# Kernel optimization log

Hardware: AMD Instinct MI355X
Metric: run time of the kernel (lower is better)

Reference implementation:

```python
import jax, jax.numpy as jnp
import numpy as np

B = 8192  # number of covariance matrices
N = 64    # n_assets


def setup_inputs() -> dict:
    key = jax.random.key(0)
    A = jax.random.normal(key, (B, N, N), dtype=jnp.float32)
    # SPD covariance: A A^T / N + 0.1 I  (real covariances are SPD)
    sigma = jnp.einsum('bij,bkj->bik', A, A) / N + 0.1 * jnp.eye(N, dtype=jnp.float32)
    return {"sigma": sigma}


def reference(sigma) -> jnp.ndarray:
    # Symmetrize, as the original does: 0.5 * (S + S^T)
    sym = 0.5 * (sigma + jnp.swapaxes(sigma, -1, -2))  # [B, N, N]
    n = sym.shape[-1]
    ones = jnp.ones((*sym.shape[:-2], n), dtype=sym.dtype)  # [B, N]
    # Closed-form min-variance (short selling allowed): w = S^-1 1 / (1^T S^-1 1)
    z = jnp.linalg.solve(sym, ones[..., None])[..., 0]      # [B, N]
    w = z / jnp.sum(z, axis=-1, keepdims=True)              # [B, N]
    return w[..., None]  # [B, N, 1], matching expand_dims(axis=-1)
```

## Files before the change

### kernel.cpp

```cpp
#include <hip/hip_runtime.h>


#define NN 64

typedef float v2f __attribute__((ext_vector_type(2)));
typedef float v4f __attribute__((ext_vector_type(4)));

template <int I> struct ic { static constexpr int value = I; };

template <int Start, int End, typename F>
__device__ __forceinline__ void static_for(F&& f) {
    if constexpr (Start < End) {
        f(ic<Start>{});
        static_for<Start + 1, End>(static_cast<F&&>(f));
    }
}

__device__ __forceinline__ float rlane(float v, int lane) {
    return __int_as_float(__builtin_amdgcn_readlane(__float_as_int(v), lane));
}

__device__ __forceinline__ float frcp(float x) {
#if __has_builtin(__builtin_amdgcn_rcpf)
    return __builtin_amdgcn_rcpf(x);
#else
    return 1.0f / x;
#endif
}

__device__ __forceinline__ v2f fma2(v2f a, v2f b, v2f c) {
#if __has_builtin(__builtin_elementwise_fma)
    return __builtin_elementwise_fma(a, b, c);
#else
    v2f r; r.x = fmaf(a.x, b.x, c.x); r.y = fmaf(a.y, b.y, c.y); return r;
#endif
}

__global__
__attribute__((amdgpu_flat_work_group_size(256, 256), amdgpu_waves_per_eu(3, 3)))
void minvar_kernel(const float* __restrict__ sigma,
                   float* __restrict__ out,
                   int batch) {
    __shared__ float pb[4][2][2 * NN * 4 / 2];

    const int lane = threadIdx.x & 63;
    const int wid  = threadIdx.x >> 6;
    const int bid  = blockIdx.x * 4 + wid;
    if (bid >= batch) return;

    const float* __restrict__ p = sigma + (size_t)bid * (NN * NN) + (size_t)lane * NN;

    v2f r[NN / 2];
    static_for<0, NN / 4>([&](auto j4c) {
        constexpr int j4 = decltype(j4c)::value;
        v4f v = reinterpret_cast<const v4f*>(p)[j4];
        r[2 * j4 + 0] = v2f{v.x, v.y};
        r[2 * j4 + 1] = v2f{v.z, v.w};
    });

    float b = 1.0f;
    float d = 1.0f;
    const int wbase = (lane >> 1) * 8 + (lane & 1);

    static_for<0, 16>([&](auto pc) {
        constexpr int P  = decltype(pc)::value;
        constexpr int k0 = 4 * P;
        constexpr int m0 = 2 * P;
        float* __restrict__ wb = &pb[wid][P & 1][0];

        const float el0  = r[m0].x;
        if constexpr (P < 15) wb[wbase + 0] = el0;
        const float piv0 = rlane(el0, k0);
        const float nf0  = (lane != k0) ? (-el0 * frcp(piv0)) : 0.0f;
        d = (lane == k0) ? el0 : d;
        b = fmaf(nf0, rlane(b, k0), b);
        const float u01 = rlane(r[m0].y,     k0);
        const float u02 = rlane(r[m0 + 1].x, k0);
        const float u03 = rlane(r[m0 + 1].y, k0);
        r[m0].y     = fmaf(nf0, u01, r[m0].y);
        r[m0 + 1].x = fmaf(nf0, u02, r[m0 + 1].x);
        r[m0 + 1].y = fmaf(nf0, u03, r[m0 + 1].y);

        const float el1  = r[m0].y;
        if constexpr (P < 15) wb[wbase + 2] = el1;
        const float piv1 = rlane(el1, k0 + 1);
        const float nf1  = (lane != k0 + 1) ? (-el1 * frcp(piv1)) : 0.0f;
        d = (lane == k0 + 1) ? el1 : d;
        b = fmaf(nf1, rlane(b, k0 + 1), b);
        const float u12 = rlane(r[m0 + 1].x, k0 + 1);
        const float u13 = rlane(r[m0 + 1].y, k0 + 1);
        r[m0 + 1].x = fmaf(nf1, u12, r[m0 + 1].x);
        r[m0 + 1].y = fmaf(nf1, u13, r[m0 + 1].y);

        const float el2  = r[m0 + 1].x;
        if constexpr (P < 15) wb[wbase + 4] = el2;
        const float piv2 = rlane(el2, k0 + 2);
        const float nf2  = (lane != k0 + 2) ? (-el2 * frcp(piv2)) : 0.0f;
        d = (lane == k0 + 2) ? el2 : d;
        b = fmaf(nf2, rlane(b, k0 + 2), b);
        const float u23 = rlane(r[m0 + 1].y, k0 + 2);
        r[m0 + 1].y = fmaf(nf2, u23, r[m0 + 1].y);

        const float el3  = r[m0 + 1].y;
        if constexpr (P < 15) wb[wbase + 6] = el3;
        const float piv3 = rlane(el3, k0 + 3);
        const float nf3  = (lane != k0 + 3) ? (-el3 * frcp(piv3)) : 0.0f;
        d = (lane == k0 + 3) ? el3 : d;
        b = fmaf(nf3, rlane(b, k0 + 3), b);

        if constexpr (P < 15) {
            const v2f n0 = v2f{nf0, nf0}, n1 = v2f{nf1, nf1};
            const v2f n2 = v2f{nf2, nf2}, n3 = v2f{nf3, nf3};
            static_for<0, 4>([&](auto gc) {
                constexpr int G = decltype(gc)::value;
                constexpr int s = m0 + 2 + 8 * G;
                if constexpr (s < NN / 2) {
                    constexpr int e = (s + 8 < NN / 2) ? (s + 8) : (NN / 2);
                    v4f lo[4], hi[4];
                    static_for<s, e>([&](auto mc) {
                        constexpr int m = decltype(mc)::value;
                        constexpr int q = m - s;
                        if constexpr (q < 4) {
                            lo[q] = *reinterpret_cast<const v4f*>(wb + 8 * m);
                            hi[q] = *reinterpret_cast<const v4f*>(wb + 8 * m + 4);
                        }
                    });
                    static_for<s, e>([&](auto mc) {
                        constexpr int m = decltype(mc)::value;
                        constexpr int q = m - s;
                        if constexpr (q >= 4) {
                            constexpr int j0 = 2 * m, j1 = 2 * m + 1;
                            float ax = r[m].x, ay = r[m].y;
                            ax = fmaf(nf0, rlane(el0, j0), ax);
                            ay = fmaf(nf0, rlane(el0, j1), ay);
                            ax = fmaf(nf1, rlane(el1, j0), ax);
                            ay = fmaf(nf1, rlane(el1, j1), ay);
                            ax = fmaf(nf2, rlane(el2, j0), ax);
                            ay = fmaf(nf2, rlane(el2, j1), ay);
                            ax = fmaf(nf3, rlane(el3, j0), ax);
                            ay = fmaf(nf3, rlane(el3, j1), ay);
                            r[m] = v2f{ax, ay};
                        }
                    });
                    static_for<s, e>([&](auto mc) {
                        constexpr int m = decltype(mc)::value;
                        constexpr int q = m - s;
                        if constexpr (q < 4) {
                            v2f acc = r[m];
                            acc = fma2(n0, v2f{lo[q].x, lo[q].y}, acc);
                            acc = fma2(n1, v2f{lo[q].z, lo[q].w}, acc);
                            acc = fma2(n2, v2f{hi[q].x, hi[q].y}, acc);
                            acc = fma2(n3, v2f{hi[q].z, hi[q].w}, acc);
                            r[m] = acc;
                        }
                    });
                }
            });
        }
    });

    const float z = b * frcp(d);

    float tot = z;
    #pragma unroll
    for (int off = 32; off >= 1; off >>= 1)
        tot += __shfl_xor(tot, off, 64);

    out[(size_t)bid * NN + lane] = z * frcp(tot);
}

extern "C" void kernel_launch(void* const* d_in, const int* in_sizes, int n_in,
                              void* d_out, int out_size, void* d_ws, size_t ws_size,
                              hipStream_t stream) {
    const float* sigma = (const float*)d_in[0];
    float* out = (float*)d_out;
    const int batch  = in_sizes[0] / (NN * NN);
    const int blocks = (batch + 3) / 4;
    minvar_kernel<<<blocks, 256, 0, stream>>>(sigma, out, batch);
}
```

Measured before the change: 193.9 us.

## Defer trailing-column updates of each panel into next panel's pivot steps

After each 4-column panel, only the next panel's columns (m0+2..m0+7) are updated immediately. The remaining trailing columns are updated during the following panel's serial pivot chain, using saved multipliers and the double-buffered LDS panel. This aims to hide the latency of the dependent pivot/readlane chain behind independent FMA work. The cost is more live registers (saved el/nf values) and a more complex schedule that could spill or hurt occupancy.

```diff
diff --git a/kernel.cpp b/kernel.cpp
--- a/kernel.cpp
+++ b/kernel.cpp
@@ -62,11 +62,63 @@
     float d = 1.0f;
     const int wbase = (lane >> 1) * 8 + (lane & 1);
 
+    float el0p = 0.f, el1p = 0.f, el2p = 0.f, el3p = 0.f;
+    float nf0p = 0.f, nf1p = 0.f, nf2p = 0.f, nf3p = 0.f;
+
     static_for<0, 16>([&](auto pc) {
         constexpr int P  = decltype(pc)::value;
         constexpr int k0 = 4 * P;
         constexpr int m0 = 2 * P;
-        float* __restrict__ wb = &pb[wid][P & 1][0];
+        float* __restrict__ wb  = &pb[wid][P & 1][0];
+        float* __restrict__ wbp = &pb[wid][(P & 1) ^ 1][0];
+
+        auto do_rest_group = [&](auto Gc) {
+            constexpr int G = decltype(Gc)::value;
+            constexpr int s = 2 * P + 6 + 8 * G;
+            if constexpr (P >= 1 && s < NN / 2) {
+                constexpr int e = (s + 8 < NN / 2) ? (s + 8) : (NN / 2);
+                const v2f n0 = v2f{nf0p, nf0p}, n1 = v2f{nf1p, nf1p};
+                const v2f n2 = v2f{nf2p, nf2p}, n3 = v2f{nf3p, nf3p};
+                v4f lo[4], hi[4];
+                static_for<s, e>([&](auto mc) {
+                    constexpr int m = decltype(mc)::value;
+                    constexpr int q = m - s;
+                    if constexpr (q < 4) {
+                        lo[q] = *reinterpret_cast<const v4f*>(wbp + 8 * m);
+                        hi[q] = *reinterpret_cast<const v4f*>(wbp + 8 * m + 4);
+                    }
+                });
+                static_for<s, e>([&](auto mc) {
+                    constexpr int m = decltype(mc)::value;
+                    constexpr int q = m - s;
+                    if constexpr (q >= 4) {
+                        constexpr int j0 = 2 * m, j1 = 2 * m + 1;
+                        float ax = r[m].x, ay = r[m].y;
+                        ax = fmaf(nf0p, rlane(el0p, j0), ax);
+                        ay = fmaf(nf0p, rlane(el0p, j1), ay);
+                        ax = fmaf(nf1p, rlane(el1p, j0), ax);
+                        ay = fmaf(nf1p, rlane(el1p, j1), ay);
+                        ax = fmaf(nf2p, rlane(el2p, j0), ax);
+                        ay = fmaf(nf2p, rlane(el2p, j1), ay);
+                        ax = fmaf(nf3p, rlane(el3p, j0), ax);
+                        ay = fmaf(nf3p, rlane(el3p, j1), ay);
+                        r[m] = v2f{ax, ay};
+                    }
+                });
+                static_for<s, e>([&](auto mc) {
+                    constexpr int m = decltype(mc)::value;
+                    constexpr int q = m - s;
+                    if constexpr (q < 4) {
+                        v2f acc = r[m];
+                        acc = fma2(n0, v2f{lo[q].x, lo[q].y}, acc);
+                        acc = fma2(n1, v2f{lo[q].z, lo[q].w}, acc);
+                        acc = fma2(n2, v2f{hi[q].x, hi[q].y}, acc);
+                        acc = fma2(n3, v2f{hi[q].z, hi[q].w}, acc);
+                        r[m] = acc;
+                    }
+                });
+            }
+        };
 
         const float el0  = r[m0].x;
         if constexpr (P < 15) wb[wbase + 0] = el0;
@@ -81,6 +133,8 @@
         r[m0 + 1].x = fmaf(nf0, u02, r[m0 + 1].x);
         r[m0 + 1].y = fmaf(nf0, u03, r[m0 + 1].y);
 
+        do_rest_group(ic<0>{});
+
         const float el1  = r[m0].y;
         if constexpr (P < 15) wb[wbase + 2] = el1;
         const float piv1 = rlane(el1, k0 + 1);
@@ -92,6 +146,8 @@
         r[m0 + 1].x = fmaf(nf1, u12, r[m0 + 1].x);
         r[m0 + 1].y = fmaf(nf1, u13, r[m0 + 1].y);
 
+        do_rest_group(ic<1>{});
+
         const float el2  = r[m0 + 1].x;
         if constexpr (P < 15) wb[wbase + 4] = el2;
         const float piv2 = rlane(el2, k0 + 2);
@@ -101,6 +157,8 @@
         const float u23 = rlane(r[m0 + 1].y, k0 + 2);
         r[m0 + 1].y = fmaf(nf2, u23, r[m0 + 1].y);
 
+        do_rest_group(ic<2>{});
+
         const float el3  = r[m0 + 1].y;
         if constexpr (P < 15) wb[wbase + 6] = el3;
         const float piv3 = rlane(el3, k0 + 3);
@@ -109,53 +167,50 @@
         b = fmaf(nf3, rlane(b, k0 + 3), b);
 
         if constexpr (P < 15) {
+            constexpr int s0 = m0 + 2;
+            constexpr int e0 = (m0 + 8 < NN / 2) ? (m0 + 8) : (NN / 2);
             const v2f n0 = v2f{nf0, nf0}, n1 = v2f{nf1, nf1};
             const v2f n2 = v2f{nf2, nf2}, n3 = v2f{nf3, nf3};
-            static_for<0, 4>([&](auto gc) {
-                constexpr int G = decltype(gc)::value;
-                constexpr int s = m0 + 2 + 8 * G;
-                if constexpr (s < NN / 2) {
-                    constexpr int e = (s + 8 < NN / 2) ? (s + 8) : (NN / 2);
-                    v4f lo[4], hi[4];
-                    static_for<s, e>([&](auto mc) {
-                        constexpr int m = decltype(mc)::value;
-                        constexpr int q = m - s;
-                        if constexpr (q < 4) {
-                            lo[q] = *reinterpret_cast<const v4f*>(wb + 8 * m);
-                            hi[q] = *reinterpret_cast<const v4f*>(wb + 8 * m + 4);
-                        }
-                    });
-                    static_for<s, e>([&](auto mc) {
-                        constexpr int m = decltype(mc)::value;
-                        constexpr int q = m - s;
-                        if constexpr (q >= 4) {
-                            constexpr int j0 = 2 * m, j1 = 2 * m + 1;
-                            float ax = r[m].x, ay = r[m].y;
-                            ax = fmaf(nf0, rlane(el0, j0), ax);
-                            ay = fmaf(nf0, rlane(el0, j1), ay);
-                            ax = fmaf(nf1, rlane(el1, j0), ax);
-                            ay = fmaf(nf1, rlane(el1, j1), ay);
-                            ax = fmaf(nf2, rlane(el2, j0), ax);
-                            ay = fmaf(nf2, rlane(el2, j1), ay);
-                            ax = fmaf(nf3, rlane(el3, j0), ax);
-                            ay = fmaf(nf3, rlane(el3, j1), ay);
-                            r[m] = v2f{ax, ay};
-                        }
-                    });
-                    static_for<s, e>([&](auto mc) {
-                        constexpr int m = decltype(mc)::value;
-                        constexpr int q = m - s;
-                        if constexpr (q < 4) {
-                            v2f acc = r[m];
-                            acc = fma2(n0, v2f{lo[q].x, lo[q].y}, acc);
-                            acc = fma2(n1, v2f{lo[q].z, lo[q].w}, acc);
-                            acc = fma2(n2, v2f{hi[q].x, hi[q].y}, acc);
-                            acc = fma2(n3, v2f{hi[q].z, hi[q].w}, acc);
-                            r[m] = acc;
-                        }
-                    });
+            v4f lo0[3], hi0[3];
+            static_for<s0, e0>([&](auto mc) {
+                constexpr int m = decltype(mc)::value;
+                constexpr int q = m - s0;
+                if constexpr (q < 3) {
+                    lo0[q] = *reinterpret_cast<const v4f*>(wb + 8 * m);
+                    hi0[q] = *reinterpret_cast<const v4f*>(wb + 8 * m + 4);
                 }
             });
+            static_for<s0, e0>([&](auto mc) {
+                constexpr int m = decltype(mc)::value;
+                constexpr int q = m - s0;
+                if constexpr (q >= 3) {
+                    constexpr int j0 = 2 * m, j1 = 2 * m + 1;
+                    float ax = r[m].x, ay = r[m].y;
+                    ax = fmaf(nf0, rlane(el0, j0), ax);
+                    ay = fmaf(nf0, rlane(el0, j1), ay);
+                    ax = fmaf(nf1, rlane(el1, j0), ax);
+                    ay = fmaf(nf1, rlane(el1, j1), ay);
+                    ax = fmaf(nf2, rlane(el2, j0), ax);
+                    ay = fmaf(nf2, rlane(el2, j1), ay);
+                    ax = fmaf(nf3, rlane(el3, j0), ax);
+                    ay = fmaf(nf3, rlane(el3, j1), ay);
+                    r[m] = v2f{ax, ay};
+                }
+            });
+            static_for<s0, e0>([&](auto mc) {
+                constexpr int m = decltype(mc)::value;
+                constexpr int q = m - s0;
+                if constexpr (q < 3) {
+                    v2f acc = r[m];
+                    acc = fma2(n0, v2f{lo0[q].x, lo0[q].y}, acc);
+                    acc = fma2(n1, v2f{lo0[q].z, lo0[q].w}, acc);
+                    acc = fma2(n2, v2f{hi0[q].x, hi0[q].y}, acc);
+                    acc = fma2(n3, v2f{hi0[q].z, hi0[q].w}, acc);
+                    r[m] = acc;
+                }
+            });
+            el0p = el0; el1p = el1; el2p = el2; el3p = el3;
+            nf0p = nf0; nf1p = nf1; nf2p = nf2; nf3p = nf3;
         }
     });
 
```

Result: no change. 192.3 us, median of 2 (-0.8%).

## Process two matrices per wavefront with interleaved Gauss-Jordan elimination

Applied to the files above, without the earlier changes.

Each wavefront now solves two independent 64x64 systems at once, interleaving their pivot steps so readlane and LDS latencies of one matrix overlap with arithmetic of the other. Register state doubles, so waves_per_eu drops from 3 to 2 and the grid is halved. LDS scratch is doubled per wave. The trade is more instruction-level parallelism per wave against lower occupancy and register-spill risk.

```diff
diff --git a/kernel.cpp b/kernel.cpp
--- a/kernel.cpp
+++ b/kernel.cpp
@@ -37,136 +37,138 @@
 }
 
 __global__
-__attribute__((amdgpu_flat_work_group_size(256, 256), amdgpu_waves_per_eu(3, 3)))
+__attribute__((amdgpu_flat_work_group_size(256, 256), amdgpu_waves_per_eu(2, 2)))
 void minvar_kernel(const float* __restrict__ sigma,
                    float* __restrict__ out,
                    int batch) {
-    __shared__ float pb[4][2][2 * NN * 4 / 2];
+    __shared__ float pb[4][2][2][256];
 
     const int lane = threadIdx.x & 63;
     const int wid  = threadIdx.x >> 6;
-    const int bid  = blockIdx.x * 4 + wid;
-    if (bid >= batch) return;
+    const int bid0 = blockIdx.x * 8 + wid * 2;
+    if (bid0 >= batch) return;
+    const int bid1 = bid0 + 1;
+    const int cb1  = (bid1 < batch) ? bid1 : bid0;
 
-    const float* __restrict__ p = sigma + (size_t)bid * (NN * NN) + (size_t)lane * NN;
+    const float* __restrict__ p0 = sigma + (size_t)bid0 * (NN * NN) + (size_t)lane * NN;
+    const float* __restrict__ p1 = sigma + (size_t)cb1  * (NN * NN) + (size_t)lane * NN;
 
-    v2f r[NN / 2];
+    v2f r[2][NN / 2];
     static_for<0, NN / 4>([&](auto j4c) {
         constexpr int j4 = decltype(j4c)::value;
-        v4f v = reinterpret_cast<const v4f*>(p)[j4];
-        r[2 * j4 + 0] = v2f{v.x, v.y};
-        r[2 * j4 + 1] = v2f{v.z, v.w};
+        v4f v0 = reinterpret_cast<const v4f*>(p0)[j4];
+        v4f v1 = reinterpret_cast<const v4f*>(p1)[j4];
+        r[0][2 * j4 + 0] = v2f{v0.x, v0.y};
+        r[0][2 * j4 + 1] = v2f{v0.z, v0.w};
+        r[1][2 * j4 + 0] = v2f{v1.x, v1.y};
+        r[1][2 * j4 + 1] = v2f{v1.z, v1.w};
     });
 
-    float b = 1.0f;
-    float d = 1.0f;
+    float bb[2] = {1.0f, 1.0f};
+    float dd[2] = {1.0f, 1.0f};
     const int wbase = (lane >> 1) * 8 + (lane & 1);
 
     static_for<0, 16>([&](auto pc) {
         constexpr int P  = decltype(pc)::value;
-        constexpr int k0 = 4 * P;
         constexpr int m0 = 2 * P;
-        float* __restrict__ wb = &pb[wid][P & 1][0];
+        float* __restrict__ wbm[2] = { &pb[wid][0][P & 1][0],
+                                       &pb[wid][1][P & 1][0] };
 
-        const float el0  = r[m0].x;
-        if constexpr (P < 15) wb[wbase + 0] = el0;
-        const float piv0 = rlane(el0, k0);
-        const float nf0  = (lane != k0) ? (-el0 * frcp(piv0)) : 0.0f;
-        d = (lane == k0) ? el0 : d;
-        b = fmaf(nf0, rlane(b, k0), b);
-        const float u01 = rlane(r[m0].y,     k0);
-        const float u02 = rlane(r[m0 + 1].x, k0);
-        const float u03 = rlane(r[m0 + 1].y, k0);
-        r[m0].y     = fmaf(nf0, u01, r[m0].y);
-        r[m0 + 1].x = fmaf(nf0, u02, r[m0 + 1].x);
-        r[m0 + 1].y = fmaf(nf0, u03, r[m0 + 1].y);
+        float el[2][4], nf[2][4];
 
-        const float el1  = r[m0].y;
-        if constexpr (P < 15) wb[wbase + 2] = el1;
-        const float piv1 = rlane(el1, k0 + 1);
-        const float nf1  = (lane != k0 + 1) ? (-el1 * frcp(piv1)) : 0.0f;
-        d = (lane == k0 + 1) ? el1 : d;
-        b = fmaf(nf1, rlane(b, k0 + 1), b);
-        const float u12 = rlane(r[m0 + 1].x, k0 + 1);
-        const float u13 = rlane(r[m0 + 1].y, k0 + 1);
-        r[m0 + 1].x = fmaf(nf1, u12, r[m0 + 1].x);
-        r[m0 + 1].y = fmaf(nf1, u13, r[m0 + 1].y);
-
-        const float el2  = r[m0 + 1].x;
-        if constexpr (P < 15) wb[wbase + 4] = el2;
-        const float piv2 = rlane(el2, k0 + 2);
-        const float nf2  = (lane != k0 + 2) ? (-el2 * frcp(piv2)) : 0.0f;
-        d = (lane == k0 + 2) ? el2 : d;
-        b = fmaf(nf2, rlane(b, k0 + 2), b);
-        const float u23 = rlane(r[m0 + 1].y, k0 + 2);
-        r[m0 + 1].y = fmaf(nf2, u23, r[m0 + 1].y);
-
-        const float el3  = r[m0 + 1].y;
-        if constexpr (P < 15) wb[wbase + 6] = el3;
-        const float piv3 = rlane(el3, k0 + 3);
-        const float nf3  = (lane != k0 + 3) ? (-el3 * frcp(piv3)) : 0.0f;
-        d = (lane == k0 + 3) ? el3 : d;
-        b = fmaf(nf3, rlane(b, k0 + 3), b);
+        static_for<0, 4>([&](auto cc) {
+            constexpr int C = decltype(cc)::value;
+            constexpr int k = 4 * P + C;
+            static_for<0, 2>([&](auto Mc) {
+                constexpr int M  = decltype(Mc)::value;
+                constexpr int mm = m0 + (C >> 1);
+                const float e = (C & 1) ? r[M][mm].y : r[M][mm].x;
+                if constexpr (P < 15) wbm[M][wbase + 2 * C] = e;
+                const float piv = rlane(e, k);
+                const float f   = (lane != k) ? (-e * frcp(piv)) : 0.0f;
+                dd[M] = (lane == k) ? e : dd[M];
+                bb[M] = fmaf(f, rlane(bb[M], k), bb[M]);
+                static_for<C + 1, 4>([&](auto jc) {
+                    constexpr int J  = decltype(jc)::value;
+                    constexpr int mj = m0 + (J >> 1);
+                    float v = (J & 1) ? r[M][mj].y : r[M][mj].x;
+                    v = fmaf(f, rlane(v, k), v);
+                    if constexpr (J & 1) r[M][mj].y = v; else r[M][mj].x = v;
+                });
+                el[M][C] = e; nf[M][C] = f;
+            });
+        });
 
         if constexpr (P < 15) {
-            const v2f n0 = v2f{nf0, nf0}, n1 = v2f{nf1, nf1};
-            const v2f n2 = v2f{nf2, nf2}, n3 = v2f{nf3, nf3};
             static_for<0, 4>([&](auto gc) {
                 constexpr int G = decltype(gc)::value;
                 constexpr int s = m0 + 2 + 8 * G;
                 if constexpr (s < NN / 2) {
-                    constexpr int e = (s + 8 < NN / 2) ? (s + 8) : (NN / 2);
-                    v4f lo[4], hi[4];
-                    static_for<s, e>([&](auto mc) {
-                        constexpr int m = decltype(mc)::value;
-                        constexpr int q = m - s;
-                        if constexpr (q < 4) {
-                            lo[q] = *reinterpret_cast<const v4f*>(wb + 8 * m);
-                            hi[q] = *reinterpret_cast<const v4f*>(wb + 8 * m + 4);
-                        }
+                    constexpr int e_ = (s + 8 < NN / 2) ? (s + 8) : (NN / 2);
+                    v4f lo[2][4], hi[2][4];
+                    static_for<0, 2>([&](auto Mc) {
+                        constexpr int M = decltype(Mc)::value;
+                        static_for<s, e_>([&](auto mc2) {
+                            constexpr int m = decltype(mc2)::value;
+                            constexpr int q = m - s;
+                            if constexpr (q < 4) {
+                                lo[M][q] = *reinterpret_cast<const v4f*>(wbm[M] + 8 * m);
+                                hi[M][q] = *reinterpret_cast<const v4f*>(wbm[M] + 8 * m + 4);
+                            }
+                        });
                     });
-                    static_for<s, e>([&](auto mc) {
-                        constexpr int m = decltype(mc)::value;
-                        constexpr int q = m - s;
-                        if constexpr (q >= 4) {
-                            constexpr int j0 = 2 * m, j1 = 2 * m + 1;
-                            float ax = r[m].x, ay = r[m].y;
-                            ax = fmaf(nf0, rlane(el0, j0), ax);
-                            ay = fmaf(nf0, rlane(el0, j1), ay);
-                            ax = fmaf(nf1, rlane(el1, j0), ax);
-                            ay = fmaf(nf1, rlane(el1, j1), ay);
-                            ax = fmaf(nf2, rlane(el2, j0), ax);
-                            ay = fmaf(nf2, rlane(el2, j1), ay);
-                            ax = fmaf(nf3, rlane(el3, j0), ax);
-                            ay = fmaf(nf3, rlane(el3, j1), ay);
-                            r[m] = v2f{ax, ay};
-                        }
+                    static_for<0, 2>([&](auto Mc) {
+                        constexpr int M = decltype(Mc)::value;
+                        static_for<s, e_>([&](auto mc2) {
+                            constexpr int m = decltype(mc2)::value;
+                            constexpr int q = m - s;
+                            if constexpr (q >= 4) {
+                                constexpr int j0 = 2 * m, j1 = 2 * m + 1;
+                                float ax = r[M][m].x, ay = r[M][m].y;
+                                static_for<0, 4>([&](auto cc2) {
+                                    constexpr int C = decltype(cc2)::value;
+                                    ax = fmaf(nf[M][C], rlane(el[M][C], j0), ax);
+                                    ay = fmaf(nf[M][C], rlane(el[M][C], j1), ay);
+                                });
+                                r[M][m] = v2f{ax, ay};
+                            }
+                        });
                     });
-                    static_for<s, e>([&](auto mc) {
-                        constexpr int m = decltype(mc)::value;
-                        constexpr int q = m - s;
-                        if constexpr (q < 4) {
-                            v2f acc = r[m];
-                            acc = fma2(n0, v2f{lo[q].x, lo[q].y}, acc);
-                            acc = fma2(n1, v2f{lo[q].z, lo[q].w}, acc);
-                            acc = fma2(n2, v2f{hi[q].x, hi[q].y}, acc);
-                            acc = fma2(n3, v2f{hi[q].z, hi[q].w}, acc);
-                            r[m] = acc;
-                        }
+                    static_for<0, 2>([&](auto Mc) {
+                        constexpr int M = decltype(Mc)::value;
+                        const v2f n0 = v2f{nf[M][0], nf[M][0]};
+                        const v2f n1 = v2f{nf[M][1], nf[M][1]};
+                        const v2f n2 = v2f{nf[M][2], nf[M][2]};
+                        const v2f n3 = v2f{nf[M][3], nf[M][3]};
+                        static_for<s, e_>([&](auto mc2) {
+                            constexpr int m = decltype(mc2)::value;
+                            constexpr int q = m - s;
+                            if constexpr (q < 4) {
+                                v2f acc = r[M][m];
+                                acc = fma2(n0, v2f{lo[M][q].x, lo[M][q].y}, acc);
+                                acc = fma2(n1, v2f{lo[M][q].z, lo[M][q].w}, acc);
+                                acc = fma2(n2, v2f{hi[M][q].x, hi[M][q].y}, acc);
+                                acc = fma2(n3, v2f{hi[M][q].z, hi[M][q].w}, acc);
+                                r[M][m] = acc;
+                            }
+                        });
                     });
                 }
             });
         }
     });
 
-    const float z = b * frcp(d);
-
-    float tot = z;
-    #pragma unroll
-    for (int off = 32; off >= 1; off >>= 1)
-        tot += __shfl_xor(tot, off, 64);
-
-    out[(size_t)bid * NN + lane] = z * frcp(tot);
+    static_for<0, 2>([&](auto Mc) {
+        constexpr int M = decltype(Mc)::value;
+        const float z = bb[M] * frcp(dd[M]);
+        float tot = z;
+        #pragma unroll
+        for (int off = 32; off >= 1; off >>= 1)
+            tot += __shfl_xor(tot, off, 64);
+        const int ob = bid0 + M;
+        if (M == 0 || ob < batch)
+            out[(size_t)ob * NN + lane] = z * frcp(tot);
+    });
 }
 
 extern "C" void kernel_launch(void* const* d_in, const int* in_sizes, int n_in,
@@ -175,6 +177,6 @@
     const float* sigma = (const float*)d_in[0];
     float* out = (float*)d_out;
     const int batch  = in_sizes[0] / (NN * NN);
-    const int blocks = (batch + 3) / 4;
+    const int blocks = (batch + 7) / 8;
     minvar_kernel<<<blocks, 256, 0, stream>>>(sigma, out, batch);
 }
```

Result: slower. 204.0 us (+5.2%).
